# Kernel optimization log

Measured on AMD Instinct MI355X. Metric: run time of the kernel, lower is better.

## Reference

```python
import jax, jax.numpy as jnp
import numpy as np

B = 32
H = 56
W = 56
C = 384
HEADS = 12
WS = 7
SS = 3
HIDDEN = 768
HD = C // HEADS
SCALE = HD ** -0.5
N = WS * WS
NW = (H // WS) * (W // WS)
EPS = 1e-5


def _rel_index():
    coords = np.stack(np.meshgrid(np.arange(WS), np.arange(WS), indexing='ij'))  # (2, ws, ws)
    cf = coords.reshape(2, -1)
    rel = cf[:, :, None] - cf[:, None, :]            # (2, N, N)
    rel = rel.transpose(1, 2, 0)                     # (N, N, 2)
    rel[..., 0] += WS - 1
    rel[..., 1] += WS - 1
    rel[..., 0] *= 2 * WS - 1
    return rel.sum(-1)                               # (N, N) int


def _attn_mask():
    img = np.zeros((H, W))
    cnt = 0
    for hs in (slice(0, -WS), slice(-WS, -SS), slice(-SS, None)):
        for ws_ in (slice(0, -WS), slice(-WS, -SS), slice(-SS, None)):
            img[hs, ws_] = cnt
            cnt += 1
    mw = img.reshape(H // WS, WS, W // WS, WS).transpose(0, 2, 1, 3).reshape(-1, N)  # (nW, N)
    am = mw[:, None, :] - mw[:, :, None]             # (nW, N, N)
    return np.where(am != 0, -100.0, 0.0).astype(np.float32)

REL_IDX = jnp.asarray(_rel_index().reshape(-1))       # (N*N,)
ATTN_MASK = jnp.asarray(_attn_mask())                 # (nW, N, N)


def layer_norm(x, w, b):
    mu = jnp.mean(x, axis=-1, keepdims=True)
    var = jnp.mean(jnp.square(x - mu), axis=-1, keepdims=True)
    return (x - mu) * jax.lax.rsqrt(var + EPS) * w + b


def window_partition(x):
    # (B, H, W, C) -> (B*nW, N, C)
    x = x.reshape(B, H // WS, WS, W // WS, WS, C)
    return x.transpose(0, 1, 3, 2, 4, 5).reshape(-1, N, C)


def window_reverse(win):
    # (B*nW, N, C) -> (B, H, W, C)
    x = win.reshape(B, H // WS, W // WS, WS, WS, C)
    return x.transpose(0, 1, 3, 2, 4, 5).reshape(B, H, W, C)


def setup_inputs() -> dict:
    key = jax.random.key(0)
    ks = jax.random.split(key, 6)
    return {
        'x': jax.random.normal(ks[0], (B, H * W, C), dtype=jnp.float32),
        'norm1_w': jnp.ones((C,), jnp.float32),
        'norm1_b': jnp.zeros((C,), jnp.float32),
        'qkv_w': jax.random.normal(ks[1], (3 * C, C), jnp.float32) * 0.02,
        'qkv_b': jnp.zeros((3 * C,), jnp.float32),
        'rpb_table': jax.random.normal(ks[2], ((2 * WS - 1) ** 2, HEADS), jnp.float32) * 0.02,
        'proj_w': jax.random.normal(ks[3], (C, C), jnp.float32) * 0.02,
        'proj_b': jnp.zeros((C,), jnp.float32),
        'norm2_w': jnp.ones((C,), jnp.float32),
        'norm2_b': jnp.zeros((C,), jnp.float32),
        'fc1_w': jax.random.normal(ks[4], (HIDDEN, C), jnp.float32) * 0.02,
        'fc1_b': jnp.zeros((HIDDEN,), jnp.float32),
        'fc2_w': jax.random.normal(ks[5], (C, HIDDEN), jnp.float32) * 0.02,
        'fc2_b': jnp.zeros((C,), jnp.float32),
    }


def reference(x, norm1_w, norm1_b, qkv_w, qkv_b, rpb_table, proj_w, proj_b,
              norm2_w, norm2_b, fc1_w, fc1_b, fc2_w, fc2_b):
    shortcut = x
    xn = layer_norm(x, norm1_w, norm1_b).reshape(B, H, W, C)
    xs = jnp.roll(xn, shift=(-SS, -SS), axis=(1, 2))
    win = window_partition(xs)                                # (B_, N, C)
    B_ = win.shape[0]

    qkv = win @ qkv_w.T + qkv_b                               # (B_, N, 3C)
    qkv = qkv.reshape(B_, N, 3, HEADS, HD).transpose(2, 0, 3, 1, 4)
    q, k, v = qkv[0], qkv[1], qkv[2]                          # (B_, h, N, hd)

    attn = jnp.einsum('bhnd,bhmd->bhnm', q * SCALE, k)        # (B_, h, N, N)
    rel_bias = rpb_table[REL_IDX].reshape(N, N, HEADS).transpose(2, 0, 1)
    attn = attn + rel_bias[None]
    attn = attn.reshape(B, NW, HEADS, N, N) + ATTN_MASK[None, :, None]
    attn = jax.nn.softmax(attn.reshape(B_, HEADS, N, N), axis=-1)

    out = jnp.einsum('bhnm,bhmd->bhnd', attn, v)
    out = out.transpose(0, 2, 1, 3).reshape(B_, N, C)
    out = out @ proj_w.T + proj_b

    xr = window_reverse(out)
    xr = jnp.roll(xr, shift=(SS, SS), axis=(1, 2)).reshape(B, H * W, C)

    x = shortcut + xr
    xm = layer_norm(x, norm2_w, norm2_b)
    h = jax.nn.gelu(xm @ fc1_w.T + fc1_b, approximate=False)
    mlp = h @ fc2_w.T + fc2_b
    return x + mlp
```

## Files before the change

### kernel.cpp

```cpp
#include <hip/hip_runtime.h>
#include <hip/hip_bf16.h>
#include <cstdint>
#include <cstddef>

typedef __attribute__((ext_vector_type(8))) short bf16x8;
typedef __attribute__((ext_vector_type(4))) float f32x4;
typedef unsigned short u16;

#define SCALE_Q 0.17677669529663687f

__device__ __forceinline__ u16 f2bf(float f) {
  __hip_bfloat16 h = __float2bfloat16(f);
  union { __hip_bfloat16 h; u16 u; } cv; cv.h = h; return cv.u;
}

__device__ __forceinline__ void gload_lds16(const void* g, void* l) {
  __builtin_amdgcn_global_load_lds(
      (const __attribute__((address_space(1))) uint32_t*)g,
      (__attribute__((address_space(3))) uint32_t*)l, 16, 0, 0);
}

__global__ void cvt_kernel(const float* __restrict__ s, u16* __restrict__ d, int n) {
  int i = blockIdx.x * 256 + threadIdx.x;
  if (i < n) d[i] = f2bf(s[i]);
}

__global__ __launch_bounds__(256) void ln1_kernel(const float* __restrict__ x,
    const float* __restrict__ w, const float* __restrict__ bia, u16* __restrict__ win) {
  int wid = threadIdx.x >> 6, l = threadIdx.x & 63;
  int tok = blockIdx.x * 4 + wid;
  int b_ = tok / 49, t = tok - b_ * 49;
  int bb = b_ >> 6, wdw = b_ & 63;
  int wh = wdw >> 3, ww = wdw & 7;
  int th = t / 7, tw = t - th * 7;
  int hh = wh * 7 + th + 3; if (hh >= 56) hh -= 56;
  int wp = ww * 7 + tw + 3; if (wp >= 56) wp -= 56;
  const float* src = x + ((size_t)bb * 3136 + hh * 56 + wp) * 384;
  float v[6]; float s = 0.f, ss = 0.f;
#pragma unroll
  for (int q = 0; q < 6; ++q) { v[q] = src[l + 64 * q]; s += v[q]; ss += v[q] * v[q]; }
#pragma unroll
  for (int m = 1; m < 64; m <<= 1) { s += __shfl_xor(s, m); ss += __shfl_xor(ss, m); }
  float mean = s * (1.f / 384.f);
  float var = ss * (1.f / 384.f) - mean * mean;
  float rstd = rsqrtf(var + 1e-5f);
  u16* dst = win + (size_t)tok * 384;
#pragma unroll
  for (int q = 0; q < 6; ++q) {
    int ci = l + 64 * q;
    dst[ci] = f2bf((v[q] - mean) * rstd * w[ci] + bia[ci]);
  }
}

__global__ __launch_bounds__(256) void ln2_kernel(const float* __restrict__ x,
    const float* __restrict__ w, const float* __restrict__ bia, u16* __restrict__ o) {
  int wid = threadIdx.x >> 6, l = threadIdx.x & 63;
  int tok = blockIdx.x * 4 + wid;
  const float* src = x + (size_t)tok * 384;
  float v[6]; float s = 0.f, ss = 0.f;
#pragma unroll
  for (int q = 0; q < 6; ++q) { v[q] = src[l + 64 * q]; s += v[q]; ss += v[q] * v[q]; }
#pragma unroll
  for (int m = 1; m < 64; m <<= 1) { s += __shfl_xor(s, m); ss += __shfl_xor(ss, m); }
  float mean = s * (1.f / 384.f);
  float var = ss * (1.f / 384.f) - mean * mean;
  float rstd = rsqrtf(var + 1e-5f);
  u16* dst = o + (size_t)tok * 384;
#pragma unroll
  for (int q = 0; q < 6; ++q) {
    int ci = l + 64 * q;
    dst[ci] = f2bf((v[q] - mean) * rstd * w[ci] + bia[ci]);
  }
}

template <int EPI>
__global__ __launch_bounds__(256) void gemm_bt(
    const u16* __restrict__ A, const u16* __restrict__ W,
    const float* __restrict__ bias, int K, int nbn,
    u16* __restrict__ outb, float* __restrict__ outf, const float* __restrict__ addsrc) {
  __shared__ u16 lsA[128 * 64];
  __shared__ u16 lsB[128 * 64];
  int bid = blockIdx.x;
  int bm = bid / nbn, bn = bid - bm * nbn;
  int m0 = bm * 128, n0 = bn * 128;
  int tid = threadIdx.x;
  int w = tid >> 6, l = tid & 63;
  int wr = w >> 1, wc = w & 1;
  int g = l >> 4, c = l & 15;
  int lr = l >> 3, lc8 = (l & 7) * 8;
  f32x4 acc[4][4] = {};
  for (int k0 = 0; k0 < K; k0 += 64) {
#pragma unroll
    for (int q = 0; q < 4; ++q) {
      int row = w * 32 + q * 8 + lr;
      gload_lds16(A + (size_t)(m0 + row) * K + k0 + lc8, &lsA[(w * 32 + q * 8) * 64]);
      gload_lds16(W + (size_t)(n0 + row) * K + k0 + lc8, &lsB[(w * 32 + q * 8) * 64]);
    }
    __syncthreads();
#pragma unroll
    for (int kk = 0; kk < 2; ++kk) {
      bf16x8 af[4], bfr[4];
#pragma unroll
      for (int i = 0; i < 4; ++i)
        af[i] = *(const bf16x8*)&lsA[(wr * 64 + i * 16 + c) * 64 + kk * 32 + g * 8];
#pragma unroll
      for (int j = 0; j < 4; ++j)
        bfr[j] = *(const bf16x8*)&lsB[(wc * 64 + j * 16 + c) * 64 + kk * 32 + g * 8];
#pragma unroll
      for (int i = 0; i < 4; ++i)
#pragma unroll
        for (int j = 0; j < 4; ++j)
          acc[i][j] = __builtin_amdgcn_mfma_f32_16x16x32_bf16(af[i], bfr[j], acc[i][j], 0, 0, 0);
    }
    __syncthreads();
  }
#pragma unroll
  for (int i = 0; i < 4; ++i) {
#pragma unroll
    for (int r = 0; r < 4; ++r) {
      int row = m0 + wr * 64 + i * 16 + 4 * g + r;
#pragma unroll
      for (int j = 0; j < 4; ++j) {
        int col = n0 + wc * 64 + j * 16 + c;
        float v = acc[i][j][r] + bias[col];
        if (EPI == 0) {
          int s = col / 384, rem = col - s * 384;
          int hd = rem >> 5, d = rem & 31;
          if (s == 0) v *= SCALE_Q;
          int b_ = row / 49, t = row - b_ * 49;
          outb[(((size_t)s * 2048 + b_) * 12 + hd) * 1568 + t * 32 + d] = f2bf(v);
        } else if (EPI == 1) {
          int b_ = row / 49, t = row - b_ * 49;
          int bb = b_ >> 6, wdw = b_ & 63;
          int wh = wdw >> 3, ww = wdw & 7;
          int th = t / 7, tw = t - th * 7;
          int hh = wh * 7 + th + 3; if (hh >= 56) hh -= 56;
          int wp = ww * 7 + tw + 3; if (wp >= 56) wp -= 56;
          size_t oi = ((size_t)bb * 3136 + hh * 56 + wp) * 384 + col;
          outf[oi] = v + addsrc[oi];
        } else if (EPI == 2) {
          float gg = 0.5f * v * (1.f + erff(v * 0.70710678118654752f));
          outb[(size_t)row * 768 + col] = f2bf(gg);
        } else {
          size_t oi = (size_t)row * 384 + col;
          outf[oi] = v + addsrc[oi];
        }
      }
    }
  }
}

__global__ __launch_bounds__(256) void attn_kernel(const u16* __restrict__ qkv,
    u16* __restrict__ outb, const float* __restrict__ rpb) {
  __shared__ u16 lsP[4][64 * 72];
  __shared__ u16 lsVT[4][32 * 72];
  int wid = threadIdx.x >> 6, l = threadIdx.x & 63;
  int pair = blockIdx.x * 4 + wid;
  int b_ = pair / 12, head = pair - b_ * 12;
  int g = l >> 4, c = l & 15;
  const size_t tstride = (size_t)2048 * 12 * 1568;
  const u16* qp = qkv + ((size_t)b_ * 12 + head) * 1568;
  const u16* kp = qp + tstride;
  const u16* vp = kp + tstride;

  bf16x8 aq[4], bk[4];
#pragma unroll
  for (int i = 0; i < 4; ++i) {
    int row = i * 16 + c; if (row > 48) row = 48;
    aq[i] = *(const bf16x8*)&qp[row * 32 + g * 8];
  }
#pragma unroll
  for (int j = 0; j < 4; ++j) {
    int row = j * 16 + c; if (row > 48) row = 48;
    bk[j] = *(const bf16x8*)&kp[row * 32 + g * 8];
  }
  f32x4 s[4][4] = {};
#pragma unroll
  for (int i = 0; i < 4; ++i)
#pragma unroll
    for (int j = 0; j < 4; ++j)
      s[i][j] = __builtin_amdgcn_mfma_f32_16x16x32_bf16(aq[i], bk[j], s[i][j], 0, 0, 0);

  u16* vt = lsVT[wid];
  for (int idx = l; idx < 32 * 72; idx += 64) vt[idx] = 0;
  for (int idx = l; idx < 49 * 32; idx += 64) {
    int t = idx >> 5, d = idx & 31;
    vt[d * 72 + t] = vp[idx];
  }

  int wdw = b_ & 63;
  int wh = wdw >> 3, ww = wdw & 7;
  int cd[4], cm[4], ridc[4]; bool cbad[4];
#pragma unroll
  for (int jn = 0; jn < 4; ++jn) {
    int col = jn * 16 + c; cbad[jn] = col > 48; if (col > 48) col = 48;
    int d7 = (col * 37) >> 8; int m7 = col - d7 * 7;
    cd[jn] = d7; cm[jn] = m7;
    int rh = (wh < 7) ? 0 : ((d7 < 4) ? 1 : 2);
    int rw = (ww < 7) ? 0 : ((m7 < 4) ? 1 : 2);
    ridc[jn] = rh * 3 + rw;
  }
  u16* pw = lsP[wid];
#pragma unroll
  for (int i = 0; i < 4; ++i) {
#pragma unroll
    for (int r = 0; r < 4; ++r) {
      int row = i * 16 + 4 * g + r;
      int rowc = row > 48 ? 48 : row;
      int rd = (rowc * 37) >> 8; int rm = rowc - rd * 7;
      int rh = (wh < 7) ? 0 : ((rd < 4) ? 1 : 2);
      int rw = (ww < 7) ? 0 : ((rm < 4) ? 1 : 2);
      int ridr = rh * 3 + rw;
      float vj[4]; float mx = -3.0e38f;
#pragma unroll
      for (int jn = 0; jn < 4; ++jn) {
        int idx = (rd - cd[jn] + 6) * 13 + (rm - cm[jn] + 6);
        float v = s[i][jn][r] + rpb[idx * 12 + head];
        if (ridr != ridc[jn]) v -= 100.f;
        if (cbad[jn]) v = -1e30f;
        vj[jn] = v; mx = fmaxf(mx, v);
      }
#pragma unroll
      for (int m = 1; m < 16; m <<= 1) mx = fmaxf(mx, __shfl_xor(mx, m));
      float sm = 0.f;
#pragma unroll
      for (int jn = 0; jn < 4; ++jn) { vj[jn] = __expf(vj[jn] - mx); sm += vj[jn]; }
#pragma unroll
      for (int m = 1; m < 16; m <<= 1) sm += __shfl_xor(sm, m);
      float rinv = 1.f / sm;
#pragma unroll
      for (int jn = 0; jn < 4; ++jn) pw[row * 72 + jn * 16 + c] = f2bf(vj[jn] * rinv);
    }
  }

  f32x4 o[4][2] = {};
#pragma unroll
  for (int kk = 0; kk < 2; ++kk) {
    bf16x8 vb[2];
#pragma unroll
    for (int n = 0; n < 2; ++n)
      vb[n] = *(const bf16x8*)&vt[(n * 16 + c) * 72 + kk * 32 + g * 8];
#pragma unroll
    for (int i = 0; i < 4; ++i) {
      bf16x8 pa = *(const bf16x8*)&pw[(i * 16 + c) * 72 + kk * 32 + g * 8];
#pragma unroll
      for (int n = 0; n < 2; ++n)
        o[i][n] = __builtin_amdgcn_mfma_f32_16x16x32_bf16(pa, vb[n], o[i][n], 0, 0, 0);
    }
  }
#pragma unroll
  for (int i = 0; i < 4; ++i) {
#pragma unroll
    for (int r = 0; r < 4; ++r) {
      int row = i * 16 + 4 * g + r;
      if (row < 49) {
#pragma unroll
        for (int n = 0; n < 2; ++n)
          outb[((size_t)b_ * 49 + row) * 384 + head * 32 + n * 16 + c] = f2bf(o[i][n][r]);
      }
    }
  }
}

extern "C" void kernel_launch(void* const* d_in, const int* in_sizes, int n_in,
                              void* d_out, int out_size, void* d_ws, size_t ws_size,
                              hipStream_t stream) {
  const float* x    = (const float*)d_in[0];
  const float* n1w  = (const float*)d_in[1];
  const float* n1b  = (const float*)d_in[2];
  const float* qkvw = (const float*)d_in[3];
  const float* qkvb = (const float*)d_in[4];
  const float* rpb  = (const float*)d_in[5];
  const float* pjw  = (const float*)d_in[6];
  const float* pjb  = (const float*)d_in[7];
  const float* n2w  = (const float*)d_in[8];
  const float* n2b  = (const float*)d_in[9];
  const float* f1w  = (const float*)d_in[10];
  const float* f1b  = (const float*)d_in[11];
  const float* f2w  = (const float*)d_in[12];
  const float* f2b  = (const float*)d_in[13];
  float* out = (float*)d_out;
  uint8_t* ws = (uint8_t*)d_ws;
  u16* wq  = (u16*)(ws + 0);
  u16* wp  = (u16*)(ws + 884736);
  u16* w1  = (u16*)(ws + 1179648);
  u16* w2  = (u16*)(ws + 1769472);
  u16* win = (u16*)(ws + 2359296);
  u16* qkv = (u16*)(ws + 79429632);
  u16* xm  = qkv;
  u16* hb  = (u16*)(ws + 156499968);

  cvt_kernel<<<dim3(1728), dim3(256), 0, stream>>>(qkvw, wq, 442368);
  cvt_kernel<<<dim3(576),  dim3(256), 0, stream>>>(pjw,  wp, 147456);
  cvt_kernel<<<dim3(1152), dim3(256), 0, stream>>>(f1w,  w1, 294912);
  cvt_kernel<<<dim3(1152), dim3(256), 0, stream>>>(f2w,  w2, 294912);

  ln1_kernel<<<dim3(25088), dim3(256), 0, stream>>>(x, n1w, n1b, win);

  gemm_bt<0><<<dim3(784 * 9), dim3(256), 0, stream>>>(win, wq, qkvb, 384, 9,
                                                      qkv, (float*)nullptr, (const float*)nullptr);
  attn_kernel<<<dim3(6144), dim3(256), 0, stream>>>(qkv, win, rpb);

  gemm_bt<1><<<dim3(784 * 3), dim3(256), 0, stream>>>(win, wp, pjb, 384, 3,
                                                      (u16*)nullptr, out, x);
  ln2_kernel<<<dim3(25088), dim3(256), 0, stream>>>(out, n2w, n2b, xm);

  gemm_bt<2><<<dim3(784 * 6), dim3(256), 0, stream>>>(xm, w1, f1b, 384, 6,
                                                      hb, (float*)nullptr, (const float*)nullptr);
  gemm_bt<3><<<dim3(784 * 3), dim3(256), 0, stream>>>(hb, w2, f2b, 768, 3,
                                                      (u16*)nullptr, out, out);
}
```

Before: 1.095 ms.

## Store GEMM operands in MFMA fragment-major layout and load directly from global

```diff
diff --git a/kernel.cpp b/kernel.cpp
--- a/kernel.cpp
+++ b/kernel.cpp
@@ -14,15 +14,19 @@
   union { __hip_bfloat16 h; u16 u; } cv; cv.h = h; return cv.u;
 }
 
-__device__ __forceinline__ void gload_lds16(const void* g, void* l) {
-  __builtin_amdgcn_global_load_lds(
-      (const __attribute__((address_space(1))) uint32_t*)g,
-      (__attribute__((address_space(3))) uint32_t*)l, 16, 0, 0);
-}
-
-__global__ void cvt_kernel(const float* __restrict__ s, u16* __restrict__ d, int n) {
-  int i = blockIdx.x * 256 + threadIdx.x;
-  if (i < n) d[i] = f2bf(s[i]);
+__global__ void cvt_frag(const float* __restrict__ s, u16* __restrict__ d,
+                         int K, int nchunk) {
+  int t = blockIdx.x * 256 + threadIdx.x;
+  if (t >= nchunk) return;
+  int r = t & 127;
+  int rest = t >> 7;
+  int k8 = rest % (K >> 3);
+  int nb = rest / (K >> 3);
+  const float* src = s + ((size_t)(nb * 128 + r)) * K + k8 * 8;
+  bf16x8 v;
+#pragma unroll
+  for (int e = 0; e < 8; ++e) v[e] = (short)f2bf(src[e]);
+  *(bf16x8*)&d[(size_t)t * 8] = v;
 }
 
 __global__ __launch_bounds__(256) void ln1_kernel(const float* __restrict__ x,
@@ -44,11 +48,12 @@
   float mean = s * (1.f / 384.f);
   float var = ss * (1.f / 384.f) - mean * mean;
   float rstd = rsqrtf(var + 1e-5f);
-  u16* dst = win + (size_t)tok * 384;
+  u16* dst = win + (size_t)(tok >> 7) * 49152 + ((tok & 127) * 8) + (l & 7)
+                 + (size_t)(l >> 3) * 1024;
 #pragma unroll
   for (int q = 0; q < 6; ++q) {
     int ci = l + 64 * q;
-    dst[ci] = f2bf((v[q] - mean) * rstd * w[ci] + bia[ci]);
+    dst[(size_t)q * 8192] = f2bf((v[q] - mean) * rstd * w[ci] + bia[ci]);
   }
 }
 
@@ -65,54 +70,46 @@
   float mean = s * (1.f / 384.f);
   float var = ss * (1.f / 384.f) - mean * mean;
   float rstd = rsqrtf(var + 1e-5f);
-  u16* dst = o + (size_t)tok * 384;
+  u16* dst = o + (size_t)(tok >> 7) * 49152 + ((tok & 127) * 8) + (l & 7)
+               + (size_t)(l >> 3) * 1024;
 #pragma unroll
   for (int q = 0; q < 6; ++q) {
     int ci = l + 64 * q;
-    dst[ci] = f2bf((v[q] - mean) * rstd * w[ci] + bia[ci]);
-  }
-}
-
-template <int EPI>
+    dst[(size_t)q * 8192] = f2bf((v[q] - mean) * rstd * w[ci] + bia[ci]);
+  }
+}
+
+template <int EPI, int K>
 __global__ __launch_bounds__(256) void gemm_bt(
-    const u16* __restrict__ A, const u16* __restrict__ W,
-    const float* __restrict__ bias, int K, int nbn,
+    const u16* __restrict__ Af, const u16* __restrict__ Bf,
+    const float* __restrict__ bias, int nbn, int nwg,
     u16* __restrict__ outb, float* __restrict__ outf, const float* __restrict__ addsrc) {
-  __shared__ u16 lsA[128 * 64];
-  __shared__ u16 lsB[128 * 64];
+  constexpr int K8 = K / 8;
   int bid = blockIdx.x;
+  bid = (bid >> 3) + (bid & 7) * (nwg >> 3);
   int bm = bid / nbn, bn = bid - bm * nbn;
   int m0 = bm * 128, n0 = bn * 128;
   int tid = threadIdx.x;
   int w = tid >> 6, l = tid & 63;
   int wr = w >> 1, wc = w & 1;
   int g = l >> 4, c = l & 15;
-  int lr = l >> 3, lc8 = (l & 7) * 8;
+  const u16* Ab = Af + (size_t)bm * K8 * 1024 + (wr * 64 + c) * 8 + (size_t)g * 1024;
+  const u16* Bb = Bf + (size_t)bn * K8 * 1024 + (wc * 64 + c) * 8 + (size_t)g * 1024;
   f32x4 acc[4][4] = {};
-  for (int k0 = 0; k0 < K; k0 += 64) {
-#pragma unroll
-    for (int q = 0; q < 4; ++q) {
-      int row = w * 32 + q * 8 + lr;
-      gload_lds16(A + (size_t)(m0 + row) * K + k0 + lc8, &lsA[(w * 32 + q * 8) * 64]);
-      gload_lds16(W + (size_t)(n0 + row) * K + k0 + lc8, &lsB[(w * 32 + q * 8) * 64]);
-    }
-    __syncthreads();
-#pragma unroll
-    for (int kk = 0; kk < 2; ++kk) {
-      bf16x8 af[4], bfr[4];
-#pragma unroll
-      for (int i = 0; i < 4; ++i)
-        af[i] = *(const bf16x8*)&lsA[(wr * 64 + i * 16 + c) * 64 + kk * 32 + g * 8];
+#pragma unroll 4
+  for (int t = 0; t < K8 / 4; ++t) {
+    bf16x8 af[4], bf[4];
+#pragma unroll
+    for (int i = 0; i < 4; ++i)
+      af[i] = *(const bf16x8*)&Ab[(size_t)t * 4096 + i * 128];
+#pragma unroll
+    for (int j = 0; j < 4; ++j)
+      bf[j] = *(const bf16x8*)&Bb[(size_t)t * 4096 + j * 128];
+#pragma unroll
+    for (int i = 0; i < 4; ++i)
 #pragma unroll
       for (int j = 0; j < 4; ++j)
-        bfr[j] = *(const bf16x8*)&lsB[(wc * 64 + j * 16 + c) * 64 + kk * 32 + g * 8];
-#pragma unroll
-      for (int i = 0; i < 4; ++i)
-#pragma unroll
-        for (int j = 0; j < 4; ++j)
-          acc[i][j] = __builtin_amdgcn_mfma_f32_16x16x32_bf16(af[i], bfr[j], acc[i][j], 0, 0, 0);
-    }
-    __syncthreads();
+        acc[i][j] = __builtin_amdgcn_mfma_f32_16x16x32_bf16(af[i], bf[j], acc[i][j], 0, 0, 0);
   }
 #pragma unroll
   for (int i = 0; i < 4; ++i) {
@@ -140,7 +137,8 @@
           outf[oi] = v + addsrc[oi];
         } else if (EPI == 2) {
           float gg = 0.5f * v * (1.f + erff(v * 0.70710678118654752f));
-          outb[(size_t)row * 768 + col] = f2bf(gg);
+          int k8o = (col >> 3);
+          outb[((size_t)(row >> 7) * 96 + k8o) * 1024 + (row & 127) * 8 + (c & 7)] = f2bf(gg);
         } else {
           size_t oi = (size_t)row * 384 + col;
           outf[oi] = v + addsrc[oi];
@@ -254,9 +252,13 @@
     for (int r = 0; r < 4; ++r) {
       int row = i * 16 + 4 * g + r;
       if (row < 49) {
-#pragma unroll
-        for (int n = 0; n < 2; ++n)
-          outb[((size_t)b_ * 49 + row) * 384 + head * 32 + n * 16 + c] = f2bf(o[i][n][r]);
+        int tok = b_ * 49 + row;
+#pragma unroll
+        for (int n = 0; n < 2; ++n) {
+          int k8 = head * 4 + n * 2 + (c >> 3);
+          outb[((size_t)(tok >> 7) * 48 + k8) * 1024 + (tok & 127) * 8 + (c & 7)] =
+              f2bf(o[i][n][r]);
+        }
       }
     }
   }
@@ -290,23 +292,23 @@
   u16* xm  = qkv;
   u16* hb  = (u16*)(ws + 156499968);
 
-  cvt_kernel<<<dim3(1728), dim3(256), 0, stream>>>(qkvw, wq, 442368);
-  cvt_kernel<<<dim3(576),  dim3(256), 0, stream>>>(pjw,  wp, 147456);
-  cvt_kernel<<<dim3(1152), dim3(256), 0, stream>>>(f1w,  w1, 294912);
-  cvt_kernel<<<dim3(1152), dim3(256), 0, stream>>>(f2w,  w2, 294912);
+  cvt_frag<<<dim3(216), dim3(256), 0, stream>>>(qkvw, wq, 384, 55296);
+  cvt_frag<<<dim3(72),  dim3(256), 0, stream>>>(pjw,  wp, 384, 18432);
+  cvt_frag<<<dim3(144), dim3(256), 0, stream>>>(f1w,  w1, 384, 36864);
+  cvt_frag<<<dim3(144), dim3(256), 0, stream>>>(f2w,  w2, 768, 36864);
 
   ln1_kernel<<<dim3(25088), dim3(256), 0, stream>>>(x, n1w, n1b, win);
 
-  gemm_bt<0><<<dim3(784 * 9), dim3(256), 0, stream>>>(win, wq, qkvb, 384, 9,
-                                                      qkv, (float*)nullptr, (const float*)nullptr);
+  gemm_bt<0, 384><<<dim3(7056), dim3(256), 0, stream>>>(win, wq, qkvb, 9, 7056,
+      qkv, (float*)nullptr, (const float*)nullptr);
   attn_kernel<<<dim3(6144), dim3(256), 0, stream>>>(qkv, win, rpb);
 
-  gemm_bt<1><<<dim3(784 * 3), dim3(256), 0, stream>>>(win, wp, pjb, 384, 3,
-                                                      (u16*)nullptr, out, x);
+  gemm_bt<1, 384><<<dim3(2352), dim3(256), 0, stream>>>(win, wp, pjb, 3, 2352,
+      (u16*)nullptr, out, x);
   ln2_kernel<<<dim3(25088), dim3(256), 0, stream>>>(out, n2w, n2b, xm);
 
-  gemm_bt<2><<<dim3(784 * 6), dim3(256), 0, stream>>>(xm, w1, f1b, 384, 6,
-                                                      hb, (float*)nullptr, (const float*)nullptr);
-  gemm_bt<3><<<dim3(784 * 3), dim3(256), 0, stream>>>(hb, w2, f2b, 768, 3,
-                                                      (u16*)nullptr, out, out);
-}
+  gemm_bt<2, 384><<<dim3(4704), dim3(256), 0, stream>>>(xm, w1, f1b, 6, 4704,
+      hb, (float*)nullptr, (const float*)nullptr);
+  gemm_bt<3, 768><<<dim3(2352), dim3(256), 0, stream>>>(hb, w2, f2b, 3, 2352,
+      (u16*)nullptr, out, out);
+}
```

After: 1.271 ms. 1.16x slower.
